# Performance work log

Hardware: AMD Instinct MI355X
Metric: run time of the kernel (lower is better)

The kernel has to match this reference:

```python
import jax, jax.numpy as jnp
import numpy as np

N_NODES = 4096
N_EDGES = 262144
D = 128
N_REL = 1000
N_ENT = 50000


def setup_inputs() -> dict:
    key = jax.random.key(0)
    ks = jax.random.split(key, 6)
    x = jax.random.normal(ks[0], (N_NODES, D), dtype=jnp.float32)
    edge_index = jax.random.randint(ks[1], (2, N_EDGES), 0, N_NODES)
    relation_id = jax.random.randint(ks[2], (N_EDGES,), 0, N_REL)
    neg_flag = jax.random.randint(ks[3], (N_EDGES,), 0, 2)
    rel_emb = jax.random.normal(ks[4], (N_REL, D), dtype=jnp.float32)
    entity_emb = jax.random.normal(ks[5], (N_ENT, D), dtype=jnp.float32)
    scale = jnp.ones((N_ENT,), dtype=jnp.float32)
    bias = jnp.zeros((N_ENT,), dtype=jnp.float32)
    return {"x": x, "edge_index": edge_index, "relation_id": relation_id,
            "neg_flag": neg_flag, "rel_emb": rel_emb, "entity_emb": entity_emb,
            "scale": scale, "bias": bias}


def reference(x, edge_index, relation_id, neg_flag, rel_emb, entity_emb, scale, bias):
    src, dst = edge_index[0], edge_index[1]
    # message: gather x_j, TransE tail estimate, sign flip for negated atoms
    neg_coef = 1.0 - 2.0 * neg_flag.astype(x.dtype)           # [E]
    msg = (x[src] + rel_emb[relation_id]) * neg_coef[:, None]  # [E, D]
    # aggregate: scatter-add into target nodes
    aggr_out = jax.ops.segment_sum(msg, dst, num_segments=x.shape[0])  # [N, D]
    # update: residual + bias/scale double-matmul through entity table
    aggr = 0.1 * x + aggr_out                                  # [N, D]
    entity_score = aggr @ entity_emb.T                          # [N, V]
    entity_score = jax.nn.relu(entity_score * scale + bias)
    out = entity_score @ entity_emb                             # [N, D]
    return out
```

## Files before the change

kernel.cpp:

```cpp
#include <hip/hip_runtime.h>
#include <stdint.h>

typedef __attribute__((ext_vector_type(8))) short short8;
typedef __attribute__((ext_vector_type(8))) unsigned short ushort8;
typedef __attribute__((ext_vector_type(4))) float f32x4;
typedef __attribute__((ext_vector_type(16))) float f32x16;
typedef __attribute__((ext_vector_type(2))) unsigned int uint2v;

#define NNODES 4096
#define NEDGES 262144
#define DIM 128
#define NENT 50000
#define NENTP 50048
#define PREPB 782
#define ETILE 32
#define NT32 1563
#define NSPLIT 24
#define BCAP 128

__device__ __forceinline__ unsigned short f2bf(float f) {
  union { __bf16 b; unsigned short u; } c;
  c.b = (__bf16)f;
  return c.u;
}

__global__ __launch_bounds__(256) void k_aggr(
    const int* __restrict__ cnt, const int* __restrict__ bucket,
    const float* __restrict__ x, const float* __restrict__ rel,
    unsigned short* __restrict__ q)
{
  __shared__ float sAcc[8 * 132];
  const int n = blockIdx.x;
  const int t = threadIdx.x;
  const int slot = t >> 5;
  const int c = t & 31;
  int deg = cnt[n]; if (deg > BCAP) deg = BCAP;
  const int base = n << 7;
  float4 a0 = make_float4(0.f, 0.f, 0.f, 0.f);
  float4 a1 = make_float4(0.f, 0.f, 0.f, 0.f);
  int i = slot;
  for (; i + 8 < deg; i += 16) {
    int p0 = bucket[base + i];
    int p1 = bucket[base + i + 8];
    float4 xv0 = reinterpret_cast<const float4*>(x)[(p0 & 4095) * 32 + c];
    float4 rv0 = reinterpret_cast<const float4*>(rel)[((p0 >> 12) & 1023) * 32 + c];
    float4 xv1 = reinterpret_cast<const float4*>(x)[(p1 & 4095) * 32 + c];
    float4 rv1 = reinterpret_cast<const float4*>(rel)[((p1 >> 12) & 1023) * 32 + c];
    float s0 = (p0 & (1 << 22)) ? -1.f : 1.f;
    float s1 = (p1 & (1 << 22)) ? -1.f : 1.f;
    a0.x += s0 * (xv0.x + rv0.x); a0.y += s0 * (xv0.y + rv0.y);
    a0.z += s0 * (xv0.z + rv0.z); a0.w += s0 * (xv0.w + rv0.w);
    a1.x += s1 * (xv1.x + rv1.x); a1.y += s1 * (xv1.y + rv1.y);
    a1.z += s1 * (xv1.z + rv1.z); a1.w += s1 * (xv1.w + rv1.w);
  }
  if (i < deg) {
    int p = bucket[base + i];
    float4 xv = reinterpret_cast<const float4*>(x)[(p & 4095) * 32 + c];
    float4 rv = reinterpret_cast<const float4*>(rel)[((p >> 12) & 1023) * 32 + c];
    float sg = (p & (1 << 22)) ? -1.f : 1.f;
    a0.x += sg * (xv.x + rv.x); a0.y += sg * (xv.y + rv.y);
    a0.z += sg * (xv.z + rv.z); a0.w += sg * (xv.w + rv.w);
  }
  a0.x += a1.x; a0.y += a1.y; a0.z += a1.z; a0.w += a1.w;
  *reinterpret_cast<float4*>(&sAcc[slot * 132 + c * 4]) = a0;
  __syncthreads();
  if (t < 128) {
    float s = 0.f;
#pragma unroll
    for (int k = 0; k < 8; ++k) s += sAcc[k * 132 + t];
    q[n * DIM + t] = f2bf(0.1f * x[n * DIM + t] + s);
  }
}

__global__ __launch_bounds__(256) void k_prep(
    const float* __restrict__ ent, const float* __restrict__ scale,
    unsigned short* __restrict__ ebf, unsigned short* __restrict__ etbf,
    const int* __restrict__ ei, const int* __restrict__ rid,
    const int* __restrict__ nf, int* __restrict__ cnt, int* __restrict__ bucket)
{
  if (blockIdx.x >= PREPB) {
    int e = (blockIdx.x - PREPB) * 256 + threadIdx.x;
    int dst = ei[NEDGES + e];
    int pos = atomicAdd(&cnt[dst], 1);
    if (pos < BCAP)
      bucket[(dst << 7) + pos] = ei[e] | (rid[e] << 12) | (nf[e] << 22);
    return;
  }
  __shared__ float sT[64 * 133];
  const int t = threadIdx.x;
  const int e0 = blockIdx.x * 64;
#pragma unroll
  for (int i = 0; i < 8; ++i) {
    int idx = i * 256 + t;
    int e = idx >> 5;
    int c4 = idx & 31;
    float4 v = make_float4(0.f, 0.f, 0.f, 0.f);
    float sc = 0.f;
    if (e0 + e < NENT) {
      v = reinterpret_cast<const float4*>(ent)[(e0 + e) * 32 + c4];
      sc = scale[e0 + e];
    }
    *reinterpret_cast<float4*>(&sT[e * 133 + c4 * 4]) = v;
    ushort4 bq;
    bq.x = f2bf(v.x * sc); bq.y = f2bf(v.y * sc);
    bq.z = f2bf(v.z * sc); bq.w = f2bf(v.w * sc);
    *reinterpret_cast<ushort4*>(&ebf[(e0 + e) * 128 + c4 * 4]) = bq;
  }
  __syncthreads();
  const int lane = t & 63;
  const int w = t >> 6;
  const int dl = lane >> 3;
  const int el = (lane & 7) * 8;
#pragma unroll
  for (int it = 0; it < 4; ++it) {
    int d = it * 32 + w * 8 + dl;
    ushort8 buf;
#pragma unroll
    for (int j = 0; j < 8; ++j) buf[j] = f2bf(sT[(el + j) * 133 + d]);
    *reinterpret_cast<ushort8*>(&etbf[d * NENTP + e0 + el]) = buf;
  }
}


__device__ __forceinline__ void gll16(const void* g, void* l) {
  __builtin_amdgcn_global_load_lds(
      (const __attribute__((address_space(1))) unsigned int*)g,
      (__attribute__((address_space(3))) unsigned int*)l, 16, 0, 0);
}

__device__ __forceinline__ unsigned cvtpk(float lo, float hi) {
  unsigned r;
  asm("v_cvt_pk_bf16_f32 %0, %1, %2" : "=v"(r) : "v"(lo), "v"(hi));
  return r;
}

__global__ __launch_bounds__(256, 3) void k_flash(
    const unsigned short* __restrict__ qg,
    const unsigned short* __restrict__ ebf,
    const unsigned short* __restrict__ etbf,
    const float* __restrict__ bias,
    float* __restrict__ out)
{
  __shared__ __align__(16) unsigned short sE[2][ETILE * 128];
  __shared__ __align__(16) unsigned short sET[2][128 * ETILE];
  __shared__ __align__(16) float sBias[2][ETILE];

  const int t = threadIdx.x;
  const int w = t >> 6;
  const int lane = t & 63;
  const int l31 = lane & 31;
  const int hi = lane >> 5;

  const int bid = blockIdx.x;
  const int xcd = bid & 7;
  const int slot = bid >> 3;
  const int ysp = xcd * 3 + (slot >> 5);
  const int xb = slot & 31;

  const int m0 = xb * 128;
  const int tile_lo = (ysp * NT32) / NSPLIT;
  const int tile_hi = ((ysp + 1) * NT32) / NSPLIT;

  const int cE = (((t & 15) ^ ((t >> 4) & 15))) * 8;
  const int rE = t >> 4;
  const int cT = (((t & 3) ^ ((t >> 4) & 3))) * 8;
  const int rT = t >> 2;

  short8 qf[8];
  {
    const unsigned short* qrow = qg + (size_t)(m0 + w * 32 + l31) * DIM + hi * 8;
#pragma unroll
    for (int kk = 0; kk < 8; ++kk)
      qf[kk] = *reinterpret_cast<const short8*>(qrow + kk * 16);
  }

  f32x16 accO[4];
#pragma unroll
  for (int td = 0; td < 4; ++td)
#pragma unroll
    for (int r = 0; r < 16; ++r) accO[td][r] = 0.f;

  {
    const int vt = tile_lo * ETILE;
#pragma unroll
    for (int i = 0; i < 2; ++i)
      gll16(ebf + (size_t)(vt + i * 16 + rE) * DIM + cE, &sE[0][(i * 256 + t) * 8]);
#pragma unroll
    for (int i = 0; i < 2; ++i)
      gll16(etbf + (size_t)(i * 64 + rT) * NENTP + vt + cT, &sET[0][(i * 256 + t) * 8]);
    if (t < ETILE) sBias[0][t] = (vt + t < NENT) ? bias[vt + t] : 0.f;
  }
  __syncthreads();

  int cur = 0;
  for (int tile = tile_lo; tile < tile_hi; ++tile) {
    if (tile + 1 < tile_hi) {
      const int vt = (tile + 1) * ETILE;
#pragma unroll
      for (int i = 0; i < 2; ++i)
        gll16(ebf + (size_t)(vt + i * 16 + rE) * DIM + cE,
              &sE[cur ^ 1][(i * 256 + t) * 8]);
#pragma unroll
      for (int i = 0; i < 2; ++i)
        gll16(etbf + (size_t)(i * 64 + rT) * NENTP + vt + cT,
              &sET[cur ^ 1][(i * 256 + t) * 8]);
      if (t < ETILE) sBias[cur ^ 1][t] = (vt + t < NENT) ? bias[vt + t] : 0.f;
    }

    const unsigned short* sEc = sE[cur];
    const float* sb = sBias[cur];
    f32x16 accA, accB;
#pragma unroll
    for (int r = 0; r < 16; ++r) { accA[r] = 0.f; accB[r] = 0.f; }

    __builtin_amdgcn_s_setprio(1);
#pragma unroll
    for (int kk = 0; kk < 4; ++kk) {
      const int colA = ((kk * 4 + hi) ^ (l31 & 15)) * 8;
      const int colB = ((kk * 4 + 2 + hi) ^ (l31 & 15)) * 8;
      short8 a0 = *reinterpret_cast<const short8*>(&sEc[l31 * 128 + colA]);
      short8 a1 = *reinterpret_cast<const short8*>(&sEc[l31 * 128 + colB]);
      accA = __builtin_amdgcn_mfma_f32_32x32x16_bf16(a0, qf[2 * kk], accA, 0, 0, 0);
      accB = __builtin_amdgcn_mfma_f32_32x32x16_bf16(a1, qf[2 * kk + 1], accB, 0, 0, 0);
    }
    __builtin_amdgcn_s_setprio(0);

    short8 F[2];
    {
      float p[16];
#pragma unroll
      for (int g = 0; g < 4; ++g) {
        f32x4 b4 = *reinterpret_cast<const f32x4*>(&sb[g * 8 + hi * 4]);
#pragma unroll
        for (int j = 0; j < 4; ++j)
          p[g * 4 + j] = fmaxf(accA[g * 4 + j] + accB[g * 4 + j] + b4[j], 0.f);
      }
      unsigned wr[8];
#pragma unroll
      for (int c2 = 0; c2 < 8; ++c2) wr[c2] = cvtpk(p[2 * c2], p[2 * c2 + 1]);
      uint2v r02 = __builtin_amdgcn_permlane32_swap(wr[0], wr[2], false, false);
      uint2v r13 = __builtin_amdgcn_permlane32_swap(wr[1], wr[3], false, false);
      uint2v r46 = __builtin_amdgcn_permlane32_swap(wr[4], wr[6], false, false);
      uint2v r57 = __builtin_amdgcn_permlane32_swap(wr[5], wr[7], false, false);
      union { unsigned u[4]; short8 s; } f0, f1;
      f0.u[0] = r02[0]; f0.u[1] = r13[0]; f0.u[2] = r02[1]; f0.u[3] = r13[1];
      f1.u[0] = r46[0]; f1.u[1] = r57[0]; f1.u[2] = r46[1]; f1.u[3] = r57[1];
      F[0] = f0.s;
      F[1] = f1.s;
    }

    const unsigned short* sTc = sET[cur];
    const int keyT = (l31 >> 2) & 3;
    __builtin_amdgcn_s_setprio(1);
#pragma unroll
    for (int ke = 0; ke < 2; ++ke) {
      const int col = ((ke * 2 + hi) ^ keyT) * 8;
#pragma unroll
      for (int td = 0; td < 4; ++td) {
        const int d = td * 32 + l31;
        short8 bT = *reinterpret_cast<const short8*>(&sTc[d * ETILE + col]);
        accO[td] = __builtin_amdgcn_mfma_f32_32x32x16_bf16(F[ke], bT, accO[td], 0, 0, 0);
      }
    }
    __builtin_amdgcn_s_setprio(0);

    __syncthreads();
    cur ^= 1;
  }

#pragma unroll
  for (int td = 0; td < 4; ++td) {
#pragma unroll
    for (int r = 0; r < 16; ++r) {
      int qrow = (r & 3) + 8 * (r >> 2) + 4 * hi;
      int row = m0 + w * 32 + qrow;
      int col = td * 32 + l31;
      atomicAdd(&out[(size_t)row * DIM + col], accO[td][r]);
    }
  }
}

extern "C" void kernel_launch(void* const* d_in, const int* in_sizes, int n_in,
                              void* d_out, int out_size, void* d_ws, size_t ws_size,
                              hipStream_t stream) {
  const float* x     = (const float*)d_in[0];
  const int*   ei    = (const int*)d_in[1];
  const int*   rid   = (const int*)d_in[2];
  const int*   nf    = (const int*)d_in[3];
  const float* rel   = (const float*)d_in[4];
  const float* ent   = (const float*)d_in[5];
  const float* scale = (const float*)d_in[6];
  const float* bias  = (const float*)d_in[7];
  float* out = (float*)d_out;

  char* ws = (char*)d_ws;
  int*            cnt    = (int*)(ws + 0);
  int*            bucket = (int*)(ws + (64u << 10));
  unsigned short* qb     = (unsigned short*)(ws + (2112u << 10));
  unsigned short* ebf    = (unsigned short*)(ws + (3136u << 10));
  unsigned short* etbf   = (unsigned short*)(ws + (3136u << 10) + (size_t)NENTP * DIM * 2);

  hipMemsetAsync(cnt, 0, NNODES * sizeof(int), stream);
  hipMemsetAsync(d_out, 0, (size_t)out_size * sizeof(float), stream);
  k_prep<<<PREPB + NEDGES / 256, 256, 0, stream>>>(ent, scale, ebf, etbf,
                                                   ei, rid, nf, cnt, bucket);
  k_aggr<<<NNODES, 256, 0, stream>>>(cnt, bucket, x, rel, qb);
  k_flash<<<NSPLIT * 32, 256, 0, stream>>>(qb, ebf, etbf, bias, out);
}
```

Measured before the change: 247.0 us.

## Triple-buffer entity tiles and software-pipeline score and output MFMA phases

```diff
diff --git a/kernel.cpp b/kernel.cpp
--- a/kernel.cpp
+++ b/kernel.cpp
@@ -141,9 +141,9 @@
     const float* __restrict__ bias,
     float* __restrict__ out)
 {
-  __shared__ __align__(16) unsigned short sE[2][ETILE * 128];
-  __shared__ __align__(16) unsigned short sET[2][128 * ETILE];
-  __shared__ __align__(16) float sBias[2][ETILE];
+  __shared__ __align__(16) unsigned short sE[3][ETILE * 128];
+  __shared__ __align__(16) unsigned short sET[3][128 * ETILE];
+  __shared__ __align__(16) float sBias[4 * ETILE];
 
   const int t = threadIdx.x;
   const int w = t >> 6;
@@ -180,40 +180,21 @@
 #pragma unroll
     for (int r = 0; r < 16; ++r) accO[td][r] = 0.f;
 
-  {
-    const int vt = tile_lo * ETILE;
-#pragma unroll
-    for (int i = 0; i < 2; ++i)
-      gll16(ebf + (size_t)(vt + i * 16 + rE) * DIM + cE, &sE[0][(i * 256 + t) * 8]);
-#pragma unroll
-    for (int i = 0; i < 2; ++i)
-      gll16(etbf + (size_t)(i * 64 + rT) * NENTP + vt + cT, &sET[0][(i * 256 + t) * 8]);
-    if (t < ETILE) sBias[0][t] = (vt + t < NENT) ? bias[vt + t] : 0.f;
-  }
-  __syncthreads();
-
-  int cur = 0;
-  for (int tile = tile_lo; tile < tile_hi; ++tile) {
-    if (tile + 1 < tile_hi) {
-      const int vt = (tile + 1) * ETILE;
-#pragma unroll
-      for (int i = 0; i < 2; ++i)
-        gll16(ebf + (size_t)(vt + i * 16 + rE) * DIM + cE,
-              &sE[cur ^ 1][(i * 256 + t) * 8]);
-#pragma unroll
-      for (int i = 0; i < 2; ++i)
-        gll16(etbf + (size_t)(i * 64 + rT) * NENTP + vt + cT,
-              &sET[cur ^ 1][(i * 256 + t) * 8]);
-      if (t < ETILE) sBias[cur ^ 1][t] = (vt + t < NENT) ? bias[vt + t] : 0.f;
-    }
-
-    const unsigned short* sEc = sE[cur];
-    const float* sb = sBias[cur];
-    f32x16 accA, accB;
+  f32x16 accA, accB;
+  short8 F[2];
+
+  auto STAGE = [&](int tile, int buf) {
+    const int vt = tile * ETILE;
+    gll16(ebf + (size_t)(vt + rE) * DIM + cE, &sE[buf][t * 8]);
+    gll16(ebf + (size_t)(vt + 16 + rE) * DIM + cE, &sE[buf][(256 + t) * 8]);
+    gll16(etbf + (size_t)rT * NENTP + vt + cT, &sET[buf][t * 8]);
+    gll16(etbf + (size_t)(64 + rT) * NENTP + vt + cT, &sET[buf][(256 + t) * 8]);
+  };
+
+  auto SPHASE = [&](int buf) {
+    const unsigned short* sEc = sE[buf];
 #pragma unroll
     for (int r = 0; r < 16; ++r) { accA[r] = 0.f; accB[r] = 0.f; }
-
-    __builtin_amdgcn_s_setprio(1);
 #pragma unroll
     for (int kk = 0; kk < 4; ++kk) {
       const int colA = ((kk * 4 + hi) ^ (l31 & 15)) * 8;
@@ -223,35 +204,35 @@
       accA = __builtin_amdgcn_mfma_f32_32x32x16_bf16(a0, qf[2 * kk], accA, 0, 0, 0);
       accB = __builtin_amdgcn_mfma_f32_32x32x16_bf16(a1, qf[2 * kk + 1], accB, 0, 0, 0);
     }
-    __builtin_amdgcn_s_setprio(0);
-
-    short8 F[2];
-    {
-      float p[16];
-#pragma unroll
-      for (int g = 0; g < 4; ++g) {
-        f32x4 b4 = *reinterpret_cast<const f32x4*>(&sb[g * 8 + hi * 4]);
-#pragma unroll
-        for (int j = 0; j < 4; ++j)
-          p[g * 4 + j] = fmaxf(accA[g * 4 + j] + accB[g * 4 + j] + b4[j], 0.f);
-      }
-      unsigned wr[8];
-#pragma unroll
-      for (int c2 = 0; c2 < 8; ++c2) wr[c2] = cvtpk(p[2 * c2], p[2 * c2 + 1]);
-      uint2v r02 = __builtin_amdgcn_permlane32_swap(wr[0], wr[2], false, false);
-      uint2v r13 = __builtin_amdgcn_permlane32_swap(wr[1], wr[3], false, false);
-      uint2v r46 = __builtin_amdgcn_permlane32_swap(wr[4], wr[6], false, false);
-      uint2v r57 = __builtin_amdgcn_permlane32_swap(wr[5], wr[7], false, false);
-      union { unsigned u[4]; short8 s; } f0, f1;
-      f0.u[0] = r02[0]; f0.u[1] = r13[0]; f0.u[2] = r02[1]; f0.u[3] = r13[1];
-      f1.u[0] = r46[0]; f1.u[1] = r57[0]; f1.u[2] = r46[1]; f1.u[3] = r57[1];
-      F[0] = f0.s;
-      F[1] = f1.s;
-    }
-
-    const unsigned short* sTc = sET[cur];
+  };
+
+  auto REPACK = [&](int r4) {
+    const float* sb = sBias + (r4 & 3) * ETILE;
+    float p[16];
+#pragma unroll
+    for (int g = 0; g < 4; ++g) {
+      f32x4 b4 = *reinterpret_cast<const f32x4*>(&sb[g * 8 + hi * 4]);
+#pragma unroll
+      for (int j = 0; j < 4; ++j)
+        p[g * 4 + j] = fmaxf(accA[g * 4 + j] + accB[g * 4 + j] + b4[j], 0.f);
+    }
+    unsigned wr[8];
+#pragma unroll
+    for (int c2 = 0; c2 < 8; ++c2) wr[c2] = cvtpk(p[2 * c2], p[2 * c2 + 1]);
+    uint2v r02 = __builtin_amdgcn_permlane32_swap(wr[0], wr[2], false, false);
+    uint2v r13 = __builtin_amdgcn_permlane32_swap(wr[1], wr[3], false, false);
+    uint2v r46 = __builtin_amdgcn_permlane32_swap(wr[4], wr[6], false, false);
+    uint2v r57 = __builtin_amdgcn_permlane32_swap(wr[5], wr[7], false, false);
+    union { unsigned u[4]; short8 s; } f0, f1;
+    f0.u[0] = r02[0]; f0.u[1] = r13[0]; f0.u[2] = r02[1]; f0.u[3] = r13[1];
+    f1.u[0] = r46[0]; f1.u[1] = r57[0]; f1.u[2] = r46[1]; f1.u[3] = r57[1];
+    F[0] = f0.s;
+    F[1] = f1.s;
+  };
+
+  auto OPHASE = [&](int buf) {
+    const unsigned short* sTc = sET[buf];
     const int keyT = (l31 >> 2) & 3;
-    __builtin_amdgcn_s_setprio(1);
 #pragma unroll
     for (int ke = 0; ke < 2; ++ke) {
       const int col = ((ke * 2 + hi) ^ keyT) * 8;
@@ -262,11 +243,68 @@
         accO[td] = __builtin_amdgcn_mfma_f32_32x32x16_bf16(F[ke], bT, accO[td], 0, 0, 0);
       }
     }
+  };
+
+  STAGE(tile_lo, 0);
+  if (tile_lo + 1 < tile_hi) STAGE(tile_lo + 1, 1);
+  if (t < ETILE) {
+#pragma unroll
+    for (int j = 0; j < 3; ++j)
+      if (tile_lo + j < tile_hi) {
+        int bi = (tile_lo + j) * ETILE + t; if (bi > NENT - 1) bi = NENT - 1;
+        sBias[j * ETILE + t] = bias[bi];
+      }
+  }
+  float bv = 0.f;
+  if (w == 0 && tile_lo + 3 < tile_hi) {
+    int bi = (tile_lo + 3) * ETILE + l31; if (bi > NENT - 1) bi = NENT - 1;
+    bv = bias[bi];
+  }
+  __syncthreads();
+  SPHASE(0);
+
+  int cur = 0;
+  for (int tile = tile_lo; tile < tile_hi - 1; ++tile) {
+    const int r = tile - tile_lo;
+    int nx = cur + 1; if (nx == 3) nx = 0;
+    int st = nx + 1; if (st == 3) st = 0;
+
+    if (w == 0) {
+      if (tile + 3 < tile_hi && t < ETILE)
+        sBias[((r + 3) & 3) * ETILE + t] = bv;
+      if (tile + 4 < tile_hi) {
+        int bi = (tile + 4) * ETILE + l31; if (bi > NENT - 1) bi = NENT - 1;
+        bv = bias[bi];
+      }
+    }
+    __builtin_amdgcn_sched_barrier(0);
+    if (tile + 2 < tile_hi) STAGE(tile + 2, st);
+    __builtin_amdgcn_sched_barrier(0);
+
+    REPACK(r);
+
+    if (w == 0 && tile + 4 < tile_hi)
+      asm volatile("s_waitcnt vmcnt(5)" ::: "memory");
+    else if (tile + 2 < tile_hi)
+      asm volatile("s_waitcnt vmcnt(4)" ::: "memory");
+    else
+      asm volatile("s_waitcnt vmcnt(0)" ::: "memory");
+    __builtin_amdgcn_sched_barrier(0);
+
+    __builtin_amdgcn_s_setprio(1);
+    SPHASE(nx);
+    OPHASE(cur);
     __builtin_amdgcn_s_setprio(0);
 
-    __syncthreads();
-    cur ^= 1;
-  }
+    asm volatile("s_waitcnt lgkmcnt(0)" ::: "memory");
+    __builtin_amdgcn_s_barrier();
+    cur = nx;
+  }
+
+  REPACK(tile_hi - 1 - tile_lo);
+  __builtin_amdgcn_s_setprio(1);
+  OPHASE(cur);
+  __builtin_amdgcn_s_setprio(0);
 
 #pragma unroll
   for (int td = 0; td < 4; ++td) {
```

New measurement: 247.0 us. About the same (-0.0%).
